# Optimization experiments

Measured on AMD Instinct MI355X. Metric: run time of the kernel, lower is better.

## Reference

```python
import jax, jax.numpy as jnp
import numpy as np

B, LC, LE, D, M = 128, 256, 1024, 256, 512
NEG = -1e9


def setup_inputs() -> dict:
    key = jax.random.key(0)
    ks = jax.random.split(key, 10)
    s = 0.02
    return {
        "criteria": jax.random.normal(ks[0], (B, LC, D), jnp.float32),
        "ehr": jax.random.normal(ks[1], (B, LE, D), jnp.float32),
        "criteria_mask": jax.random.randint(ks[2], (B, LC), 0, 2, jnp.int32),
        "ehr_mask": jax.random.randint(ks[3], (B, LE), 0, 2, jnp.int32),
        # params stored (in, out); torch Linear is x @ W.T + b
        "Wa": jax.random.normal(ks[4], (D, D), jnp.float32) * s,
        "ba": jnp.zeros((D,), jnp.float32),
        "Wr": jax.random.normal(ks[5], (2 * D, D), jnp.float32) * s,
        "br": jnp.zeros((D,), jnp.float32),
        "Wm": jax.random.normal(ks[6], (4 * D, M), jnp.float32) * s,
        "bm": jnp.zeros((M,), jnp.float32),
        "Wo": jax.random.normal(ks[7], (M, 3), jnp.float32) * s,
        "bo": jnp.zeros((3,), jnp.float32),
    }


def reference(criteria, ehr, Wa, ba, Wr, br, Wm, bm, Wo, bo,
              criteria_mask, ehr_mask):
    relu = jax.nn.relu
    c = relu(criteria @ Wa + ba)              # (B, Lc, D)
    e = relu(ehr @ Wa + ba)                   # (B, Le, D)
    align = jnp.einsum("bld,bed->ble", c, e)  # (B, Lc, Le)

    cm = criteria_mask.astype(align.dtype)
    em = ehr_mask.astype(align.dtype)
    # beta: softmax over Lc (dim=1), masked by criteria_mask along Lc
    beta = jax.nn.softmax(align + (1.0 - cm)[:, :, None] * NEG, axis=1)
    # alpha: softmax over Le (dim=1 of transposed), masked by ehr_mask along Le
    alpha = jax.nn.softmax(align + (1.0 - em)[:, None, :] * NEG, axis=2)

    # (alpha.unsqueeze(-1) * ehr.unsqueeze(1)).sum(2) == alpha @ ehr
    att_c = jnp.einsum("ble,bed->bld", alpha, ehr)        # (B, Lc, D)
    r1 = relu(jnp.concatenate([att_c, criteria], axis=-1) @ Wr + br).sum(axis=1)  # (B, D)

    # (beta.unsqueeze(-1) * criteria.unsqueeze(2)).sum(1) == beta.T @ criteria
    att_e = jnp.einsum("ble,bld->bed", beta, criteria)    # (B, Le, D)
    r2 = relu(jnp.concatenate([att_e, ehr], axis=-1) @ Wr + br).sum(axis=1)       # (B, D)

    m = jnp.concatenate([r1, r2, r1 * r2, r1 - r2], axis=-1)  # (B, 4D)
    return relu(m @ Wm + bm) @ Wo + bo                        # (B, 3)
```

## Files before the change

### kernel.cpp

```cpp
#include <hip/hip_runtime.h>
#include <hip/hip_bf16.h>

#define BB 128
#define LC 256
#define LE 1024
#define DD 256
#define MM 512

typedef short bf16x8 __attribute__((ext_vector_type(8)));
typedef unsigned short u16x8 __attribute__((ext_vector_type(8)));
typedef unsigned short u16x4 __attribute__((ext_vector_type(4)));
typedef float f32x4 __attribute__((ext_vector_type(4)));

__device__ __forceinline__ float bfu2f(unsigned short u) {
  return __uint_as_float(((unsigned int)u) << 16);
}
__device__ __forceinline__ unsigned short f2bfu(float f) {
  unsigned int x = __float_as_uint(f);
  return (unsigned short)((x + 0x7fffu + ((x >> 16) & 1u)) >> 16);
}

#define LDST 40
__device__ __forceinline__ int ldsoff(int r, int q) {
  return r * LDST + ((q ^ ((r >> 2) & 3)) << 3);
}

__device__ __forceinline__ void mma_step(const unsigned short* As, const unsigned short* Bs,
                                         f32x4 (&acc)[4][4], int wm, int wn, int lane) {
  const int lm = lane & 15, quad = lane >> 4;
  bf16x8 a[4], b[4];
#pragma unroll
  for (int i = 0; i < 4; ++i) {
    int r = wm * 64 + i * 16 + lm;
    a[i] = *(const bf16x8*)&As[ldsoff(r, quad)];
    int n = wn * 64 + i * 16 + lm;
    b[i] = *(const bf16x8*)&Bs[ldsoff(n, quad)];
  }
#pragma unroll
  for (int i = 0; i < 4; ++i)
#pragma unroll
    for (int j = 0; j < 4; ++j)
      acc[i][j] = __builtin_amdgcn_mfma_f32_16x16x32_bf16(a[i], b[j], acc[i][j], 0, 0, 0);
}

__device__ __forceinline__ void stage_bf16(unsigned short* S, const unsigned short* g,
                                           long ld, int tid) {
#pragma unroll
  for (int i = 0; i < 2; ++i) {
    int c = tid + i * 256;
    int r = c >> 2, q = c & 3;
    u16x8 v = *(const u16x8*)(g + (long)r * ld + q * 8);
    *(u16x8*)&S[ldsoff(r, q)] = v;
  }
}

__device__ __forceinline__ void stage_f32(unsigned short* S, const float* g, long ld, int tid) {
#pragma unroll
  for (int i = 0; i < 2; ++i) {
    int c = tid + i * 256;
    int r = c >> 2, q = c & 3;
    const float4* p = (const float4*)(g + (long)r * ld + q * 8);
    float4 v0 = p[0], v1 = p[1];
    u16x8 o;
    o[0] = f2bfu(v0.x); o[1] = f2bfu(v0.y); o[2] = f2bfu(v0.z); o[3] = f2bfu(v0.w);
    o[4] = f2bfu(v1.x); o[5] = f2bfu(v1.y); o[6] = f2bfu(v1.z); o[7] = f2bfu(v1.w);
    *(u16x8*)&S[ldsoff(r, q)] = o;
  }
}

__global__ void zero_kernel(float* __restrict__ p, int n) {
  int i = blockIdx.x * 256 + threadIdx.x;
  if (i < n) p[i] = 0.f;
}

__global__ void wconv_kernel(const float* __restrict__ Wa, const float* __restrict__ Wr,
                             unsigned short* __restrict__ WaT, unsigned short* __restrict__ WrT) {
  int i = blockIdx.x * 256 + threadIdx.x;
  if (i < 65536) WaT[i] = f2bfu(Wa[(i & 255) * 256 + (i >> 8)]);
  if (i < 131072) WrT[i] = f2bfu(Wr[(long)(i & 511) * 256 + (i >> 9)]);
}

__global__ void transT_kernel(const float* __restrict__ src, const int* __restrict__ mask,
                              unsigned short* __restrict__ dstT, unsigned short* __restrict__ dstN,
                              int R, int C) {
  __shared__ unsigned short T[64][72];
  const int tid = threadIdx.x, b = blockIdx.z;
  const int r0 = blockIdx.y * 64, c0 = blockIdx.x * 64;
  const float* s = src + (long)b * R * C;
  const int* mk = mask + (long)b * R;
  unsigned short* dT = dstT + (long)b * R * C;
  unsigned short* dN = dstN + (long)b * R * C;
#pragma unroll
  for (int i = 0; i < 4; ++i) {
    int r = (tid >> 4) + i * 16, c4 = tid & 15;
    float4 v = *(const float4*)(s + (long)(r0 + r) * C + c0 + c4 * 4);
    u16x4 nat;
    nat[0] = f2bfu(v.x); nat[1] = f2bfu(v.y); nat[2] = f2bfu(v.z); nat[3] = f2bfu(v.w);
    *(u16x4*)(dN + (long)(r0 + r) * C + c0 + c4 * 4) = nat;
    float g = mk[r0 + r] ? 1.f : 0.f;
    T[c4 * 4 + 0][r] = f2bfu(v.x * g);
    T[c4 * 4 + 1][r] = f2bfu(v.y * g);
    T[c4 * 4 + 2][r] = f2bfu(v.z * g);
    T[c4 * 4 + 3][r] = f2bfu(v.w * g);
  }
  __syncthreads();
#pragma unroll
  for (int j = 0; j < 2; ++j) {
    int idx = tid * 2 + j;
    int row = idx >> 3, ch = idx & 7;
    *(u16x8*)(dT + (long)(c0 + row) * R + r0 + ch * 8) = *(const u16x8*)&T[row][ch * 8];
  }
}

__global__ __launch_bounds__(256, 2) void proj_mfma(const float* __restrict__ A,
                                                    const unsigned short* __restrict__ WaT,
                                                    const float* __restrict__ ba,
                                                    unsigned short* __restrict__ out) {
  __shared__ unsigned short As[128 * LDST], Bs[128 * LDST];
  const int tid = threadIdx.x, lane = tid & 63, w = tid >> 6, wm = w >> 1, wn = w & 1;
  const long m0 = (long)blockIdx.y * 128;
  const int n0 = blockIdx.x * 128;
  f32x4 acc[4][4] = {};
  for (int k0 = 0; k0 < DD; k0 += 32) {
    stage_f32(As, A + m0 * DD + k0, DD, tid);
    stage_bf16(Bs, WaT + (long)n0 * DD + k0, DD, tid);
    __syncthreads();
    mma_step(As, Bs, acc, wm, wn, lane);
    __syncthreads();
  }
  const int lm = lane & 15, quad = lane >> 4;
#pragma unroll
  for (int i = 0; i < 4; ++i)
#pragma unroll
    for (int j = 0; j < 4; ++j) {
      int col = n0 + wn * 64 + j * 16 + lm;
      float bias = ba[col];
#pragma unroll
      for (int r = 0; r < 4; ++r) {
        long row = m0 + wm * 64 + i * 16 + quad * 4 + r;
        float v = acc[i][j][r] + bias;
        out[row * DD + col] = f2bfu(v > 0.f ? v : 0.f);
      }
    }
}

__global__ __launch_bounds__(256, 2) void align_fused(
    const unsigned short* __restrict__ cB, const unsigned short* __restrict__ eB,
    const int* __restrict__ em, const int* __restrict__ cm,
    unsigned short* __restrict__ expv, unsigned short* __restrict__ expvT,
    float* __restrict__ asum, float* __restrict__ bsum) {
  __shared__ unsigned short As[128 * LDST], Bs[128 * LDST];
  __shared__ float asum_s[128], bsum_s[128];
  const int tid = threadIdx.x, lane = tid & 63, w = tid >> 6, wm = w >> 1, wn = w & 1;
  const int b = blockIdx.z, m0 = blockIdx.y * 128, n0 = blockIdx.x * 128;
  const unsigned short* Ag = cB + ((long)b * LC + m0) * DD;
  const unsigned short* Bg = eB + ((long)b * LE + n0) * DD;
  f32x4 acc[4][4] = {};
  for (int k0 = 0; k0 < DD; k0 += 32) {
    stage_bf16(As, Ag + k0, DD, tid);
    stage_bf16(Bs, Bg + k0, DD, tid);
    __syncthreads();
    mma_step(As, Bs, acc, wm, wn, lane);
    __syncthreads();
  }
  if (tid < 128) { asum_s[tid] = 0.f; bsum_s[tid] = 0.f; }
  __syncthreads();
  const int lm = lane & 15, quad = lane >> 4;
  float emv[4], cmv[4][4];
#pragma unroll
  for (int j = 0; j < 4; ++j)
    emv[j] = em[b * LE + n0 + wn * 64 + j * 16 + lm] ? 1.f : 0.f;
#pragma unroll
  for (int i = 0; i < 4; ++i)
#pragma unroll
    for (int r = 0; r < 4; ++r)
      cmv[i][r] = cm[b * LC + m0 + wm * 64 + i * 16 + quad * 4 + r] ? 1.f : 0.f;
#pragma unroll
  for (int i = 0; i < 4; ++i)
#pragma unroll
    for (int j = 0; j < 4; ++j) {
      int col = n0 + wn * 64 + j * 16 + lm;
      int lrow0 = m0 + wm * 64 + i * 16 + quad * 4;
      u16x4 tv;
#pragma unroll
      for (int r = 0; r < 4; ++r) {
        float e_ = __expf(acc[i][j][r]);
        acc[i][j][r] = e_;
        unsigned short bv = f2bfu(e_);
        expv[((long)b * LC + lrow0 + r) * LE + col] = bv;
        tv[r] = bv;
      }
      *(u16x4*)&expvT[((long)b * LE + col) * LC + lrow0] = tv;
    }
#pragma unroll
  for (int i = 0; i < 4; ++i)
#pragma unroll
    for (int r = 0; r < 4; ++r) {
      float s = emv[0] * acc[i][0][r] + emv[1] * acc[i][1][r] +
                emv[2] * acc[i][2][r] + emv[3] * acc[i][3][r];
      s += __shfl_xor(s, 1); s += __shfl_xor(s, 2);
      s += __shfl_xor(s, 4); s += __shfl_xor(s, 8);
      if (lm == 0) atomicAdd(&asum_s[wm * 64 + i * 16 + quad * 4 + r], s);
    }
#pragma unroll
  for (int j = 0; j < 4; ++j) {
    float t = 0.f;
#pragma unroll
    for (int i = 0; i < 4; ++i)
#pragma unroll
      for (int r = 0; r < 4; ++r) t += cmv[i][r] * acc[i][j][r];
    t += __shfl_xor(t, 16); t += __shfl_xor(t, 32);
    if (quad == 0) atomicAdd(&bsum_s[wn * 64 + j * 16 + lm], t);
  }
  __syncthreads();
  if (tid < 128) {
    atomicAdd(&asum[b * LC + m0 + tid], asum_s[tid]);
    atomicAdd(&bsum[b * LE + n0 + tid], bsum_s[tid]);
  }
}

__global__ __launch_bounds__(256, 2) void attc_mfma(const unsigned short* __restrict__ expv,
                                                    const unsigned short* __restrict__ ehrTm,
                                                    const float* __restrict__ asum,
                                                    unsigned short* __restrict__ attc) {
  __shared__ unsigned short As[128 * LDST], Bs[128 * LDST];
  const int tid = threadIdx.x, lane = tid & 63, w = tid >> 6, wm = w >> 1, wn = w & 1;
  const int b = blockIdx.z, m0 = blockIdx.y * 128, n0 = blockIdx.x * 128;
  const unsigned short* Ag = expv + ((long)b * LC + m0) * LE;
  const unsigned short* Bg = ehrTm + ((long)b * DD + n0) * LE;
  f32x4 acc[4][4] = {};
  for (int k0 = 0; k0 < LE; k0 += 32) {
    stage_bf16(As, Ag + k0, LE, tid);
    stage_bf16(Bs, Bg + k0, LE, tid);
    __syncthreads();
    mma_step(As, Bs, acc, wm, wn, lane);
    __syncthreads();
  }
  const int lm = lane & 15, quad = lane >> 4;
  float rs[4][4];
#pragma unroll
  for (int i = 0; i < 4; ++i)
#pragma unroll
    for (int r = 0; r < 4; ++r)
      rs[i][r] = 1.f / asum[b * LC + m0 + wm * 64 + i * 16 + quad * 4 + r];
#pragma unroll
  for (int i = 0; i < 4; ++i)
#pragma unroll
    for (int j = 0; j < 4; ++j) {
      int col = n0 + wn * 64 + j * 16 + lm;
#pragma unroll
      for (int r = 0; r < 4; ++r) {
        int row = m0 + wm * 64 + i * 16 + quad * 4 + r;
        attc[((long)b * LC + row) * DD + col] = f2bfu(acc[i][j][r] * rs[i][r]);
      }
    }
}

__global__ __launch_bounds__(256, 2) void atte_mfma(const unsigned short* __restrict__ expvT,
                                                    const unsigned short* __restrict__ critTm,
                                                    const float* __restrict__ bsum,
                                                    unsigned short* __restrict__ atte) {
  __shared__ unsigned short As[128 * LDST], Bs[128 * LDST];
  const int tid = threadIdx.x, lane = tid & 63, w = tid >> 6, wm = w >> 1, wn = w & 1;
  const int b = blockIdx.z, m0 = blockIdx.y * 128, n0 = blockIdx.x * 128;
  const unsigned short* Ag = expvT + ((long)b * LE + m0) * LC;
  const unsigned short* Bg = critTm + ((long)b * DD + n0) * LC;
  f32x4 acc[4][4] = {};
  for (int k0 = 0; k0 < LC; k0 += 32) {
    stage_bf16(As, Ag + k0, LC, tid);
    stage_bf16(Bs, Bg + k0, LC, tid);
    __syncthreads();
    mma_step(As, Bs, acc, wm, wn, lane);
    __syncthreads();
  }
  const int lm = lane & 15, quad = lane >> 4;
  float rs[4][4];
#pragma unroll
  for (int i = 0; i < 4; ++i)
#pragma unroll
    for (int r = 0; r < 4; ++r)
      rs[i][r] = 1.f / bsum[b * LE + m0 + wm * 64 + i * 16 + quad * 4 + r];
#pragma unroll
  for (int i = 0; i < 4; ++i)
#pragma unroll
    for (int j = 0; j < 4; ++j) {
      int col = n0 + wn * 64 + j * 16 + lm;
#pragma unroll
      for (int r = 0; r < 4; ++r) {
        int row = m0 + wm * 64 + i * 16 + quad * 4 + r;
        atte[((long)b * LE + row) * DD + col] = f2bfu(acc[i][j][r] * rs[i][r]);
      }
    }
}

__global__ __launch_bounds__(256, 2) void rsum_mfma(const unsigned short* __restrict__ att,
                                                    const unsigned short* __restrict__ origB,
                                                    const unsigned short* __restrict__ WrT,
                                                    const float* __restrict__ br,
                                                    float* __restrict__ rout, int Lseq) {
  __shared__ unsigned short As[128 * LDST], Bs[128 * LDST];
  __shared__ float red[2][128];
  const int tid = threadIdx.x, lane = tid & 63, w = tid >> 6, wm = w >> 1, wn = w & 1;
  const long m0 = (long)blockIdx.y * 128;
  const int n0 = blockIdx.x * 128;
  const int b = (int)(m0 / Lseq);
  f32x4 acc[4][4] = {};
  for (int k0 = 0; k0 < 2 * DD; k0 += 32) {
    if (k0 < DD)
      stage_bf16(As, att + m0 * DD + k0, DD, tid);
    else
      stage_bf16(As, origB + m0 * DD + (k0 - DD), DD, tid);
    stage_bf16(Bs, WrT + (long)n0 * (2 * DD) + k0, 2 * DD, tid);
    __syncthreads();
    mma_step(As, Bs, acc, wm, wn, lane);
    __syncthreads();
  }
  const int lm = lane & 15, quad = lane >> 4;
#pragma unroll
  for (int j = 0; j < 4; ++j) {
    int col = n0 + wn * 64 + j * 16 + lm;
    float bias = br[col];
    float s = 0.f;
#pragma unroll
    for (int i = 0; i < 4; ++i)
#pragma unroll
      for (int r = 0; r < 4; ++r) {
        float v = acc[i][j][r] + bias;
        s += v > 0.f ? v : 0.f;
      }
    s += __shfl_xor(s, 16);
    s += __shfl_xor(s, 32);
    if (quad == 0) red[wm][wn * 64 + j * 16 + lm] = s;
  }
  __syncthreads();
  if (tid < 128)
    atomicAdd(&rout[b * DD + n0 + tid], red[0][tid] + red[1][tid]);
}

__global__ void mbuild_kernel(const float* __restrict__ r1, const float* __restrict__ r2,
                              unsigned short* __restrict__ mB) {
  int i = blockIdx.x * 256 + threadIdx.x;
  int b = i >> 8, d = i & 255;
  float v1 = r1[i], v2 = r2[i];
  unsigned short* row = mB + (long)b * 1024;
  row[d] = f2bfu(v1);
  row[256 + d] = f2bfu(v2);
  row[512 + d] = f2bfu(v1 * v2);
  row[768 + d] = f2bfu(v1 - v2);
}

__global__ __launch_bounds__(256, 2) void mlp_mfma(const unsigned short* __restrict__ mB,
                                                   const float* __restrict__ Wm,
                                                   const float* __restrict__ bm,
                                                   float* __restrict__ h) {
  __shared__ unsigned short As[128 * LDST], Bs[128 * LDST];
  const int tid = threadIdx.x, lane = tid & 63, w = tid >> 6, wm = w >> 1, wn = w & 1;
  const int n0 = blockIdx.x * 128;
  f32x4 acc[4][4] = {};
  for (int k0 = 0; k0 < 4 * DD; k0 += 32) {
    stage_bf16(As, mB + k0, 4 * DD, tid);
    {
      const int dcc = tid & 7, er = tid >> 3;
#pragma unroll
      for (int i = 0; i < 4; ++i) {
        int nch = dcc + i * 8;
        float4 v = *(const float4*)(Wm + (long)(k0 + er) * MM + n0 + nch * 4);
        float vv[4] = {v.x, v.y, v.z, v.w};
#pragma unroll
        for (int q = 0; q < 4; ++q)
          Bs[ldsoff(nch * 4 + q, er >> 3) + (er & 7)] = f2bfu(vv[q]);
      }
    }
    __syncthreads();
    mma_step(As, Bs, acc, wm, wn, lane);
    __syncthreads();
  }
  const int lm = lane & 15, quad = lane >> 4;
#pragma unroll
  for (int i = 0; i < 4; ++i)
#pragma unroll
    for (int j = 0; j < 4; ++j) {
      int col = n0 + wn * 64 + j * 16 + lm;
      float bias = bm[col];
#pragma unroll
      for (int r = 0; r < 4; ++r) {
        int row = wm * 64 + i * 16 + quad * 4 + r;
        float v = acc[i][j][r] + bias;
        h[(long)row * MM + col] = v > 0.f ? v : 0.f;
      }
    }
}

__global__ void out3_kernel(const float* __restrict__ h, const float* __restrict__ Wo,
                            const float* __restrict__ bo, float* __restrict__ out) {
  const int b = blockIdx.x, tid = threadIdx.x;
  __shared__ float red[256];
  float a[3] = {0.f, 0.f, 0.f};
  for (int k = tid; k < MM; k += 256) {
    float hv = h[(long)b * MM + k];
    a[0] += hv * Wo[k * 3 + 0];
    a[1] += hv * Wo[k * 3 + 1];
    a[2] += hv * Wo[k * 3 + 2];
  }
#pragma unroll
  for (int o = 0; o < 3; ++o) {
    red[tid] = a[o]; __syncthreads();
    for (int st = 128; st > 0; st >>= 1) {
      if (tid < st) red[tid] += red[tid + st];
      __syncthreads();
    }
    if (tid == 0) out[b * 3 + o] = red[0] + bo[o];
    __syncthreads();
  }
}

extern "C" void kernel_launch(void* const* d_in, const int* in_sizes, int n_in,
                              void* d_out, int out_size, void* d_ws, size_t ws_size,
                              hipStream_t stream) {
  const float* criteria = (const float*)d_in[0];
  const float* ehr      = (const float*)d_in[1];
  const int*   cmask    = (const int*)d_in[2];
  const int*   emask    = (const int*)d_in[3];
  const float* Wa       = (const float*)d_in[4];
  const float* ba       = (const float*)d_in[5];
  const float* Wr       = (const float*)d_in[6];
  const float* br       = (const float*)d_in[7];
  const float* Wm       = (const float*)d_in[8];
  const float* bm       = (const float*)d_in[9];
  const float* Wo       = (const float*)d_in[10];
  const float* bo       = (const float*)d_in[11];
  float* out = (float*)d_out;

  char* ws = (char*)d_ws;
  unsigned short* cB     = (unsigned short*)(ws);
  unsigned short* eB     = (unsigned short*)(ws + 16777216);
  unsigned short* alignB = (unsigned short*)(ws + 83886080);
  unsigned short* ehrTm  = (unsigned short*)(ws + 150994944);
  unsigned short* critTm = (unsigned short*)(ws + 218103808);
  unsigned short* expvT  = (unsigned short*)(ws + 234881024);
  unsigned short* ehrN   = (unsigned short*)(ws + 301989888);
  unsigned short* critN  = (unsigned short*)(ws + 369098752);
  float* asum = (float*)(ws + 385875968);
  float* bsum = (float*)(ws + 386007040);
  float* r1   = (float*)(ws + 386531328);
  float* r2   = (float*)(ws + 386662400);
  unsigned short* WaT = (unsigned short*)(ws + 386793472);
  unsigned short* WrT = (unsigned short*)(ws + 386924544);
  unsigned short* mB  = (unsigned short*)(ws + 387186688);
  float* hbuf         = (float*)(ws + 387448832);
  unsigned short* attc  = cB;
  unsigned short* atteP = alignB;

  dim3 blk(256);
  zero_kernel<<<dim3(896), blk, 0, stream>>>(asum, 229376);
  wconv_kernel<<<dim3(512), blk, 0, stream>>>(Wa, Wr, WaT, WrT);
  transT_kernel<<<dim3(DD / 64, LE / 64, BB), blk, 0, stream>>>(ehr, emask, ehrTm, ehrN, LE, DD);
  transT_kernel<<<dim3(DD / 64, LC / 64, BB), blk, 0, stream>>>(criteria, cmask, critTm, critN, LC, DD);
  proj_mfma<<<dim3(2, (BB * LC) / 128), blk, 0, stream>>>(criteria, WaT, ba, cB);
  proj_mfma<<<dim3(2, (BB * LE) / 128), blk, 0, stream>>>(ehr, WaT, ba, eB);
  align_fused<<<dim3(LE / 128, LC / 128, BB), blk, 0, stream>>>(cB, eB, emask, cmask,
                                                                alignB, expvT, asum, bsum);
  attc_mfma<<<dim3(DD / 128, LC / 128, BB), blk, 0, stream>>>(alignB, ehrTm, asum, attc);
  atte_mfma<<<dim3(DD / 128, LE / 128, BB), blk, 0, stream>>>(expvT, critTm, bsum, atteP);
  rsum_mfma<<<dim3(2, (BB * LC) / 128), blk, 0, stream>>>(attc, critN, WrT, br, r1, LC);
  rsum_mfma<<<dim3(2, (BB * LE) / 128), blk, 0, stream>>>(atteP, ehrN, WrT, br, r2, LE);
  mbuild_kernel<<<dim3(BB), blk, 0, stream>>>(r1, r2, mB);
  mlp_mfma<<<dim3(MM / 128), blk, 0, stream>>>(mB, Wm, bm, hbuf);
  out3_kernel<<<dim3(BB), blk, 0, stream>>>(hbuf, Wo, bo, out);
}
```

Before: 625.2 us.

## Fuse alignment, exp and attention matmuls into flash-style per-row kernels

```diff
diff --git a/kernel.cpp b/kernel.cpp
--- a/kernel.cpp
+++ b/kernel.cpp
@@ -40,6 +40,24 @@
   for (int i = 0; i < 4; ++i)
 #pragma unroll
     for (int j = 0; j < 4; ++j)
+      acc[i][j] = __builtin_amdgcn_mfma_f32_16x16x32_bf16(a[i], b[j], acc[i][j], 0, 0, 0);
+}
+
+template <int MT, int NT>
+__device__ __forceinline__ void mma_tiles(const unsigned short* As, const unsigned short* Bs,
+                                          f32x4 (&acc)[MT][NT], int m0, int n0, int lane) {
+  const int lm = lane & 15, quad = lane >> 4;
+  bf16x8 a[MT], b[NT];
+#pragma unroll
+  for (int i = 0; i < MT; ++i)
+    a[i] = *(const bf16x8*)&As[ldsoff(m0 + i * 16 + lm, quad)];
+#pragma unroll
+  for (int j = 0; j < NT; ++j)
+    b[j] = *(const bf16x8*)&Bs[ldsoff(n0 + j * 16 + lm, quad)];
+#pragma unroll
+  for (int i = 0; i < MT; ++i)
+#pragma unroll
+    for (int j = 0; j < NT; ++j)
       acc[i][j] = __builtin_amdgcn_mfma_f32_16x16x32_bf16(a[i], b[j], acc[i][j], 0, 0, 0);
 }
 
@@ -65,6 +83,22 @@
     o[0] = f2bfu(v0.x); o[1] = f2bfu(v0.y); o[2] = f2bfu(v0.z); o[3] = f2bfu(v0.w);
     o[4] = f2bfu(v1.x); o[5] = f2bfu(v1.y); o[6] = f2bfu(v1.z); o[7] = f2bfu(v1.w);
     *(u16x8*)&S[ldsoff(r, q)] = o;
+  }
+}
+
+__device__ __forceinline__ void stage512(unsigned short* S, const unsigned short* g,
+                                         long ld, int tid) {
+  int r = tid >> 2, q = tid & 3;
+  *(u16x8*)&S[ldsoff(r, q)] = *(const u16x8*)(g + (long)r * ld + q * 8);
+}
+
+__device__ __forceinline__ void stage512x2(unsigned short* S, const unsigned short* g,
+                                           long ld, int tid) {
+#pragma unroll
+  for (int it = 0; it < 2; ++it) {
+    int c = tid + it * 512;
+    int r = c >> 2, q = c & 3;
+    *(u16x8*)&S[ldsoff(r, q)] = *(const u16x8*)(g + (long)r * ld + q * 8);
   }
 }
 
@@ -144,151 +178,180 @@
     }
 }
 
-__global__ __launch_bounds__(256, 2) void align_fused(
+__global__ __launch_bounds__(512, 2) void attn_c_fused(
     const unsigned short* __restrict__ cB, const unsigned short* __restrict__ eB,
-    const int* __restrict__ em, const int* __restrict__ cm,
-    unsigned short* __restrict__ expv, unsigned short* __restrict__ expvT,
-    float* __restrict__ asum, float* __restrict__ bsum) {
-  __shared__ unsigned short As[128 * LDST], Bs[128 * LDST];
-  __shared__ float asum_s[128], bsum_s[128];
-  const int tid = threadIdx.x, lane = tid & 63, w = tid >> 6, wm = w >> 1, wn = w & 1;
-  const int b = blockIdx.z, m0 = blockIdx.y * 128, n0 = blockIdx.x * 128;
+    const unsigned short* __restrict__ ehrTm, const int* __restrict__ em,
+    unsigned short* __restrict__ attc) {
+  __shared__ unsigned short AB[256 * LDST];
+  __shared__ unsigned short S4[4][128 * LDST];
+  __shared__ float asum_s[128];
+  const int tid = threadIdx.x, lane = tid & 63, w = tid >> 6;
+  const int lm = lane & 15, quad = lane >> 4;
+  const int wmS = w >> 2, wnS = w & 3;
+  const int wm = w >> 2, wn = w & 3;
+  const int fid = blockIdx.x;
+  const int lid = (fid & 7) * 32 + (fid >> 3);
+  const int b = lid >> 1, m0 = (lid & 1) * 128;
+  unsigned short* As = AB;
+  unsigned short* Bs = AB + 128 * LDST;
   const unsigned short* Ag = cB + ((long)b * LC + m0) * DD;
-  const unsigned short* Bg = eB + ((long)b * LE + n0) * DD;
+  if (tid < 128) asum_s[tid] = 0.f;
   f32x4 acc[4][4] = {};
-  for (int k0 = 0; k0 < DD; k0 += 32) {
-    stage_bf16(As, Ag + k0, DD, tid);
-    stage_bf16(Bs, Bg + k0, DD, tid);
-    __syncthreads();
-    mma_step(As, Bs, acc, wm, wn, lane);
-    __syncthreads();
-  }
-  if (tid < 128) { asum_s[tid] = 0.f; bsum_s[tid] = 0.f; }
+  float ap0 = 0.f, ap1 = 0.f;
   __syncthreads();
-  const int lm = lane & 15, quad = lane >> 4;
-  float emv[4], cmv[4][4];
-#pragma unroll
-  for (int j = 0; j < 4; ++j)
-    emv[j] = em[b * LE + n0 + wn * 64 + j * 16 + lm] ? 1.f : 0.f;
+  for (int ch = 0; ch < 8; ++ch) {
+    const unsigned short* Eg = eB + ((long)b * LE + ch * 128) * DD;
+    f32x4 accS[4][2] = {};
+    for (int k0 = 0; k0 < DD; k0 += 32) {
+      stage512(As, Eg + k0, DD, tid);
+      stage512(Bs, Ag + k0, DD, tid);
+      __syncthreads();
+      mma_tiles<4, 2>(As, Bs, accS, wmS * 64, wnS * 32, lane);
+      __syncthreads();
+    }
+#pragma unroll
+    for (int i = 0; i < 4; ++i) {
+      const int Le0 = wmS * 64 + i * 16 + quad * 4;
+      const int4 m4 = *(const int4*)(em + (long)b * LE + ch * 128 + Le0);
+      const float em0 = m4.x ? 1.f : 0.f, em1 = m4.y ? 1.f : 0.f;
+      const float em2 = m4.z ? 1.f : 0.f, em3 = m4.w ? 1.f : 0.f;
+      const int kk = Le0 >> 5, wi = Le0 & 31;
+      const int qq = wi >> 3, sub = wi & 7;
+#pragma unroll
+      for (int j = 0; j < 2; ++j) {
+        const int row = wnS * 32 + j * 16 + lm;
+        float e0 = __expf(accS[i][j][0]);
+        float e1 = __expf(accS[i][j][1]);
+        float e2 = __expf(accS[i][j][2]);
+        float e3 = __expf(accS[i][j][3]);
+        float s = em0 * e0 + em1 * e1 + em2 * e2 + em3 * e3;
+        if (j == 0) ap0 += s; else ap1 += s;
+        u16x4 pk;
+        pk[0] = f2bfu(e0); pk[1] = f2bfu(e1); pk[2] = f2bfu(e2); pk[3] = f2bfu(e3);
+        *(u16x4*)&S4[kk][ldsoff(row, qq) + sub] = pk;
+      }
+    }
+    __syncthreads();
+    for (int kk = 0; kk < 4; ++kk) {
+      stage512x2(AB, ehrTm + (long)b * DD * LE + ch * 128 + kk * 32, LE, tid);
+      __syncthreads();
+      mma_tiles<4, 4>(&S4[kk][0], AB, acc, wm * 64, wn * 64, lane);
+      __syncthreads();
+    }
+  }
+  {
+    float s = ap0;
+    s += __shfl_xor(s, 16); s += __shfl_xor(s, 32);
+    if (quad == 0) atomicAdd(&asum_s[wnS * 32 + 0 * 16 + lm], s);
+    float t = ap1;
+    t += __shfl_xor(t, 16); t += __shfl_xor(t, 32);
+    if (quad == 0) atomicAdd(&asum_s[wnS * 32 + 1 * 16 + lm], t);
+  }
+  __syncthreads();
+  float rs[4][4];
 #pragma unroll
   for (int i = 0; i < 4; ++i)
 #pragma unroll
     for (int r = 0; r < 4; ++r)
-      cmv[i][r] = cm[b * LC + m0 + wm * 64 + i * 16 + quad * 4 + r] ? 1.f : 0.f;
+      rs[i][r] = 1.f / asum_s[wm * 64 + i * 16 + quad * 4 + r];
 #pragma unroll
   for (int i = 0; i < 4; ++i)
 #pragma unroll
     for (int j = 0; j < 4; ++j) {
-      int col = n0 + wn * 64 + j * 16 + lm;
-      int lrow0 = m0 + wm * 64 + i * 16 + quad * 4;
-      u16x4 tv;
+      int col = wn * 64 + j * 16 + lm;
 #pragma unroll
       for (int r = 0; r < 4; ++r) {
-        float e_ = __expf(acc[i][j][r]);
-        acc[i][j][r] = e_;
-        unsigned short bv = f2bfu(e_);
-        expv[((long)b * LC + lrow0 + r) * LE + col] = bv;
-        tv[r] = bv;
-      }
-      *(u16x4*)&expvT[((long)b * LE + col) * LC + lrow0] = tv;
-    }
-#pragma unroll
-  for (int i = 0; i < 4; ++i)
-#pragma unroll
-    for (int r = 0; r < 4; ++r) {
-      float s = emv[0] * acc[i][0][r] + emv[1] * acc[i][1][r] +
-                emv[2] * acc[i][2][r] + emv[3] * acc[i][3][r];
-      s += __shfl_xor(s, 1); s += __shfl_xor(s, 2);
-      s += __shfl_xor(s, 4); s += __shfl_xor(s, 8);
-      if (lm == 0) atomicAdd(&asum_s[wm * 64 + i * 16 + quad * 4 + r], s);
-    }
-#pragma unroll
-  for (int j = 0; j < 4; ++j) {
-    float t = 0.f;
-#pragma unroll
-    for (int i = 0; i < 4; ++i)
-#pragma unroll
-      for (int r = 0; r < 4; ++r) t += cmv[i][r] * acc[i][j][r];
+        int row = wm * 64 + i * 16 + quad * 4 + r;
+        attc[((long)b * LC + m0 + row) * DD + col] = f2bfu(acc[i][j][r] * rs[i][r]);
+      }
+    }
+}
+
+__global__ __launch_bounds__(512, 2) void attn_e_fused(
+    const unsigned short* __restrict__ cB, const unsigned short* __restrict__ eB,
+    const unsigned short* __restrict__ critTm, const int* __restrict__ cm,
+    unsigned short* __restrict__ atte) {
+  __shared__ unsigned short AB[256 * LDST];
+  __shared__ unsigned short S4[4][128 * LDST];
+  __shared__ float bsum_s[128];
+  const int tid = threadIdx.x, lane = tid & 63, w = tid >> 6;
+  const int lm = lane & 15, quad = lane >> 4;
+  const int wmS = w >> 2, wnS = w & 3;
+  const int wm = w >> 2, wn = w & 3;
+  const int fid = blockIdx.x;
+  const int lid = (fid & 7) * 128 + (fid >> 3);
+  const int b = lid >> 3, n0 = (lid & 7) * 128;
+  unsigned short* As = AB;
+  unsigned short* Bs = AB + 128 * LDST;
+  const unsigned short* Eg = eB + ((long)b * LE + n0) * DD;
+  if (tid < 128) bsum_s[tid] = 0.f;
+  f32x4 acc[4][4] = {};
+  float bp0 = 0.f, bp1 = 0.f;
+  __syncthreads();
+  for (int ch = 0; ch < 2; ++ch) {
+    const unsigned short* Cg = cB + ((long)b * LC + ch * 128) * DD;
+    f32x4 accS[4][2] = {};
+    for (int k0 = 0; k0 < DD; k0 += 32) {
+      stage512(As, Cg + k0, DD, tid);
+      stage512(Bs, Eg + k0, DD, tid);
+      __syncthreads();
+      mma_tiles<4, 2>(As, Bs, accS, wmS * 64, wnS * 32, lane);
+      __syncthreads();
+    }
+#pragma unroll
+    for (int i = 0; i < 4; ++i) {
+      const int Lc0 = wmS * 64 + i * 16 + quad * 4;
+      const int4 m4 = *(const int4*)(cm + (long)b * LC + ch * 128 + Lc0);
+      const float cm0 = m4.x ? 1.f : 0.f, cm1 = m4.y ? 1.f : 0.f;
+      const float cm2 = m4.z ? 1.f : 0.f, cm3 = m4.w ? 1.f : 0.f;
+      const int kk = Lc0 >> 5, wi = Lc0 & 31;
+      const int qq = wi >> 3, sub = wi & 7;
+#pragma unroll
+      for (int j = 0; j < 2; ++j) {
+        const int row = wnS * 32 + j * 16 + lm;
+        float e0 = __expf(accS[i][j][0]);
+        float e1 = __expf(accS[i][j][1]);
+        float e2 = __expf(accS[i][j][2]);
+        float e3 = __expf(accS[i][j][3]);
+        float s = cm0 * e0 + cm1 * e1 + cm2 * e2 + cm3 * e3;
+        if (j == 0) bp0 += s; else bp1 += s;
+        u16x4 pk;
+        pk[0] = f2bfu(e0); pk[1] = f2bfu(e1); pk[2] = f2bfu(e2); pk[3] = f2bfu(e3);
+        *(u16x4*)&S4[kk][ldsoff(row, qq) + sub] = pk;
+      }
+    }
+    __syncthreads();
+    for (int kk = 0; kk < 4; ++kk) {
+      stage512x2(AB, critTm + (long)b * DD * LC + ch * 128 + kk * 32, LC, tid);
+      __syncthreads();
+      mma_tiles<4, 4>(&S4[kk][0], AB, acc, wm * 64, wn * 64, lane);
+      __syncthreads();
+    }
+  }
+  {
+    float s = bp0;
+    s += __shfl_xor(s, 16); s += __shfl_xor(s, 32);
+    if (quad == 0) atomicAdd(&bsum_s[wnS * 32 + 0 * 16 + lm], s);
+    float t = bp1;
     t += __shfl_xor(t, 16); t += __shfl_xor(t, 32);
-    if (quad == 0) atomicAdd(&bsum_s[wn * 64 + j * 16 + lm], t);
+    if (quad == 0) atomicAdd(&bsum_s[wnS * 32 + 1 * 16 + lm], t);
   }
   __syncthreads();
-  if (tid < 128) {
-    atomicAdd(&asum[b * LC + m0 + tid], asum_s[tid]);
-    atomicAdd(&bsum[b * LE + n0 + tid], bsum_s[tid]);
-  }
-}
-
-__global__ __launch_bounds__(256, 2) void attc_mfma(const unsigned short* __restrict__ expv,
-                                                    const unsigned short* __restrict__ ehrTm,
-                                                    const float* __restrict__ asum,
-                                                    unsigned short* __restrict__ attc) {
-  __shared__ unsigned short As[128 * LDST], Bs[128 * LDST];
-  const int tid = threadIdx.x, lane = tid & 63, w = tid >> 6, wm = w >> 1, wn = w & 1;
-  const int b = blockIdx.z, m0 = blockIdx.y * 128, n0 = blockIdx.x * 128;
-  const unsigned short* Ag = expv + ((long)b * LC + m0) * LE;
-  const unsigned short* Bg = ehrTm + ((long)b * DD + n0) * LE;
-  f32x4 acc[4][4] = {};
-  for (int k0 = 0; k0 < LE; k0 += 32) {
-    stage_bf16(As, Ag + k0, LE, tid);
-    stage_bf16(Bs, Bg + k0, LE, tid);
-    __syncthreads();
-    mma_step(As, Bs, acc, wm, wn, lane);
-    __syncthreads();
-  }
-  const int lm = lane & 15, quad = lane >> 4;
   float rs[4][4];
 #pragma unroll
   for (int i = 0; i < 4; ++i)
 #pragma unroll
     for (int r = 0; r < 4; ++r)
-      rs[i][r] = 1.f / asum[b * LC + m0 + wm * 64 + i * 16 + quad * 4 + r];
+      rs[i][r] = 1.f / bsum_s[wm * 64 + i * 16 + quad * 4 + r];
 #pragma unroll
   for (int i = 0; i < 4; ++i)
 #pragma unroll
     for (int j = 0; j < 4; ++j) {
-      int col = n0 + wn * 64 + j * 16 + lm;
+      int col = wn * 64 + j * 16 + lm;
 #pragma unroll
       for (int r = 0; r < 4; ++r) {
-        int row = m0 + wm * 64 + i * 16 + quad * 4 + r;
-        attc[((long)b * LC + row) * DD + col] = f2bfu(acc[i][j][r] * rs[i][r]);
-      }
-    }
-}
-
-__global__ __launch_bounds__(256, 2) void atte_mfma(const unsigned short* __restrict__ expvT,
-                                                    const unsigned short* __restrict__ critTm,
-                                                    const float* __restrict__ bsum,
-                                                    unsigned short* __restrict__ atte) {
-  __shared__ unsigned short As[128 * LDST], Bs[128 * LDST];
-  const int tid = threadIdx.x, lane = tid & 63, w = tid >> 6, wm = w >> 1, wn = w & 1;
-  const int b = blockIdx.z, m0 = blockIdx.y * 128, n0 = blockIdx.x * 128;
-  const unsigned short* Ag = expvT + ((long)b * LE + m0) * LC;
-  const unsigned short* Bg = critTm + ((long)b * DD + n0) * LC;
-  f32x4 acc[4][4] = {};
-  for (int k0 = 0; k0 < LC; k0 += 32) {
-    stage_bf16(As, Ag + k0, LC, tid);
-    stage_bf16(Bs, Bg + k0, LC, tid);
-    __syncthreads();
-    mma_step(As, Bs, acc, wm, wn, lane);
-    __syncthreads();
-  }
-  const int lm = lane & 15, quad = lane >> 4;
-  float rs[4][4];
-#pragma unroll
-  for (int i = 0; i < 4; ++i)
-#pragma unroll
-    for (int r = 0; r < 4; ++r)
-      rs[i][r] = 1.f / bsum[b * LE + m0 + wm * 64 + i * 16 + quad * 4 + r];
-#pragma unroll
-  for (int i = 0; i < 4; ++i)
-#pragma unroll
-    for (int j = 0; j < 4; ++j) {
-      int col = n0 + wn * 64 + j * 16 + lm;
-#pragma unroll
-      for (int r = 0; r < 4; ++r) {
-        int row = m0 + wm * 64 + i * 16 + quad * 4 + r;
-        atte[((long)b * LE + row) * DD + col] = f2bfu(acc[i][j][r] * rs[i][r]);
+        int row = wm * 64 + i * 16 + quad * 4 + r;
+        atte[((long)b * LE + n0 + row) * DD + col] = f2bfu(acc[i][j][r] * rs[i][r]);
       }
     }
 }
@@ -434,34 +497,28 @@
   char* ws = (char*)d_ws;
   unsigned short* cB     = (unsigned short*)(ws);
   unsigned short* eB     = (unsigned short*)(ws + 16777216);
-  unsigned short* alignB = (unsigned short*)(ws + 83886080);
-  unsigned short* ehrTm  = (unsigned short*)(ws + 150994944);
-  unsigned short* critTm = (unsigned short*)(ws + 218103808);
-  unsigned short* expvT  = (unsigned short*)(ws + 234881024);
-  unsigned short* ehrN   = (unsigned short*)(ws + 301989888);
-  unsigned short* critN  = (unsigned short*)(ws + 369098752);
-  float* asum = (float*)(ws + 385875968);
-  float* bsum = (float*)(ws + 386007040);
-  float* r1   = (float*)(ws + 386531328);
-  float* r2   = (float*)(ws + 386662400);
-  unsigned short* WaT = (unsigned short*)(ws + 386793472);
-  unsigned short* WrT = (unsigned short*)(ws + 386924544);
-  unsigned short* mB  = (unsigned short*)(ws + 387186688);
-  float* hbuf         = (float*)(ws + 387448832);
-  unsigned short* attc  = cB;
-  unsigned short* atteP = alignB;
+  unsigned short* ehrTm  = (unsigned short*)(ws + 83886080);
+  unsigned short* critTm = (unsigned short*)(ws + 150994944);
+  unsigned short* ehrN   = (unsigned short*)(ws + 167772160);
+  unsigned short* critN  = (unsigned short*)(ws + 234881024);
+  unsigned short* attc   = (unsigned short*)(ws + 251658240);
+  unsigned short* atteP  = (unsigned short*)(ws + 268435456);
+  float* r1   = (float*)(ws + 335544320);
+  float* r2   = (float*)(ws + 335675392);
+  unsigned short* WaT = (unsigned short*)(ws + 335806464);
+  unsigned short* WrT = (unsigned short*)(ws + 335937536);
+  unsigned short* mB  = (unsigned short*)(ws + 336199680);
+  float* hbuf         = (float*)(ws + 336461824);
 
   dim3 blk(256);
-  zero_kernel<<<dim3(896), blk, 0, stream>>>(asum, 229376);
+  zero_kernel<<<dim3(256), blk, 0, stream>>>(r1, 65536);
   wconv_kernel<<<dim3(512), blk, 0, stream>>>(Wa, Wr, WaT, WrT);
   transT_kernel<<<dim3(DD / 64, LE / 64, BB), blk, 0, stream>>>(ehr, emask, ehrTm, ehrN, LE, DD);
   transT_kernel<<<dim3(DD / 64, LC / 64, BB), blk, 0, stream>>>(criteria, cmask, critTm, critN, LC, DD);
   proj_mfma<<<dim3(2, (BB * LC) / 128), blk, 0, stream>>>(criteria, WaT, ba, cB);
   proj_mfma<<<dim3(2, (BB * LE) / 128), blk, 0, stream>>>(ehr, WaT, ba, eB);
-  align_fused<<<dim3(LE / 128, LC / 128, BB), blk, 0, stream>>>(cB, eB, emask, cmask,
-                                                                alignB, expvT, asum, bsum);
-  attc_mfma<<<dim3(DD / 128, LC / 128, BB), blk, 0, stream>>>(alignB, ehrTm, asum, attc);
-  atte_mfma<<<dim3(DD / 128, LE / 128, BB), blk, 0, stream>>>(expvT, critTm, bsum, atteP);
+  attn_c_fused<<<dim3(BB * (LC / 128)), dim3(512), 0, stream>>>(cB, eB, ehrTm, emask, attc);
+  attn_e_fused<<<dim3(BB * (LE / 128)), dim3(512), 0, stream>>>(cB, eB, critTm, cmask, atteP);
   rsum_mfma<<<dim3(2, (BB * LC) / 128), blk, 0, stream>>>(attc, critN, WrT, br, r1, LC);
   rsum_mfma<<<dim3(2, (BB * LE) / 128), blk, 0, stream>>>(atteP, ehrN, WrT, br, r2, LE);
   mbuild_kernel<<<dim3(BB), blk, 0, stream>>>(r1, r2, mB);
```

New measurement: 623.9 us. No clear change (-0.2%).
